# Kernel tuning notes

Measured on AMD Instinct MI355X. Metric: run time of the kernel, lower is better.

The kernel has to match this reference:

```python
import jax, jax.numpy as jnp
import numpy as np

B, S, N = 1024, 64, 256
ODE_UNFOLDS = 12
EPS = 1e-8
ELAPSED_TIME = 1.0

def _uniform(key, shape, lo, hi):
    return jax.random.uniform(key, shape, jnp.float32, lo, hi)

def setup_inputs() -> dict:
    key = jax.random.key(0)
    ks = jax.random.split(key, 16)
    return {
        "inputs": jax.random.normal(ks[0], (B, S), jnp.float32),
        "state": jax.random.normal(ks[1], (B, N), jnp.float32),
        "gleak": _uniform(ks[2], (N,), 0.001, 1.0),
        "vleak": _uniform(ks[3], (N,), -0.2, 0.2),
        "cm": _uniform(ks[4], (N,), 0.4, 0.6),
        "w": _uniform(ks[5], (N, N), 0.001, 1.0),
        "sigma": _uniform(ks[6], (N, N), 3.0, 8.0),
        "mu": _uniform(ks[7], (N, N), 0.3, 0.8),
        "erev": jnp.where(jax.random.bernoulli(ks[8], 0.5, (N, N)), 1.0, -1.0).astype(jnp.float32),
        "sensory_w": _uniform(ks[9], (S, N), 0.001, 1.0),
        "sensory_sigma": _uniform(ks[10], (S, N), 3.0, 8.0),
        "sensory_mu": _uniform(ks[11], (S, N), 0.3, 0.8),
        "sensory_erev": jnp.where(jax.random.bernoulli(ks[12], 0.5, (S, N)), 1.0, -1.0).astype(jnp.float32),
        "sparsity_mask": jax.random.bernoulli(ks[13], 0.5, (N, N)).astype(jnp.float32),
        "sensory_sparsity_mask": jax.random.bernoulli(ks[14], 0.5, (S, N)).astype(jnp.float32),
    }

def _sig(v_pre, mu, sigma):
    # v_pre: [B, pre] -> [B, pre, 1]; mu/sigma: [pre, post] -> broadcast to [B, pre, post]
    return jax.nn.sigmoid(sigma[None] * (v_pre[:, :, None] - mu[None]))

def reference(inputs, state, gleak, vleak, cm, w, sigma, mu, erev,
              sensory_w, sensory_sigma, sensory_mu, sensory_erev,
              sparsity_mask, sensory_sparsity_mask):
    # sensory pre-activation (computed once): [B, S, N]
    sensory_act = jax.nn.softplus(sensory_w) * _sig(inputs, sensory_mu, sensory_sigma)
    sensory_act = sensory_act * sensory_sparsity_mask
    w_num_sensory = jnp.sum(sensory_act * sensory_erev, axis=1)  # [B, N]
    w_den_sensory = jnp.sum(sensory_act, axis=1)                 # [B, N]

    cm_t = jax.nn.softplus(cm) / (ELAPSED_TIME / ODE_UNFOLDS)    # [N]
    w_param = jax.nn.softplus(w)                                 # [N, N]
    gleak_sp = jax.nn.softplus(gleak)                            # [N]

    def step(v_pre, _):
        w_act = w_param * _sig(v_pre, mu, sigma) * sparsity_mask  # [B, N, N]
        w_num = jnp.sum(w_act * erev, axis=1) + w_num_sensory     # [B, N]
        w_den = jnp.sum(w_act, axis=1) + w_den_sensory            # [B, N]
        numerator = cm_t * v_pre + gleak_sp * vleak + w_num
        denominator = cm_t + gleak_sp + w_den
        return numerator / (denominator + EPS), None

    v_pre, _ = jax.lax.scan(step, state, None, length=ODE_UNFOLDS)
    return v_pre
```

## Files before the change

kernel.cpp:

```cpp
#include <hip/hip_runtime.h>
#include <math.h>

#define B_TOT   1024
#define S_DIM   64
#define N_DIM   256
#define UNFOLDS 12
#define EPSF    1e-8f
#define L2E     1.4426950408889634f
#define KMAX    256
#define ECLAMP  1073741824.0f

#if defined(__has_builtin)
#  if __has_builtin(__builtin_amdgcn_exp2f)
#    define FEXP2(x) __builtin_amdgcn_exp2f(x)
#  endif
#  if __has_builtin(__builtin_amdgcn_rcpf)
#    define FRCP(x) __builtin_amdgcn_rcpf(x)
#  endif
#endif
#ifndef FEXP2
__device__ __forceinline__ float __fexp2_asm(float x){ float r; asm("v_exp_f32 %0, %1" : "=v"(r) : "v"(x)); return r; }
#  define FEXP2(x) __fexp2_asm(x)
#endif
#ifndef FRCP
__device__ __forceinline__ float __frcp_asm(float x){ float r; asm("v_rcp_f32 %0, %1" : "=v"(r) : "v"(x)); return r; }
#  define FRCP(x) __frcp_asm(x)
#endif

__device__ __forceinline__ float softplus_f(float x) {
    return log1pf(expf(x));
}

#define MQUAD(p, v0, v1, v2, v3, m0, d0, m1, d1, m2, d2, m3, d3)            \
    {                                                                       \
        float _t0 = fmaf(p.x, v0, p.y);                                     \
        float _t1 = fmaf(p.x, v1, p.y);                                     \
        float _t2 = fmaf(p.x, v2, p.y);                                     \
        float _t3 = fmaf(p.x, v3, p.y);                                     \
        float _e0 = fminf(FEXP2(_t0), ECLAMP);                              \
        float _e1 = fminf(FEXP2(_t1), ECLAMP);                              \
        float _e2 = fminf(FEXP2(_t2), ECLAMP);                              \
        float _e3 = fminf(FEXP2(_t3), ECLAMP);                              \
        float _a0 = 1.0f + _e0, _a1 = 1.0f + _e1;                           \
        float _a2 = 1.0f + _e2, _a3 = 1.0f + _e3;                           \
        float _b01 = _a0 * _a1, _b23 = _a2 * _a3;                           \
        float _ip   = FRCP(_b01 * _b23);                                    \
        float _ip01 = _b23 * _ip, _ip23 = _b01 * _ip;                       \
        float _r0 = _a1 * _ip01, _r1 = _a0 * _ip01;                         \
        float _r2 = _a3 * _ip23, _r3 = _a2 * _ip23;                         \
        m0 = fmaf(p.w, _r0, m0); d0 = fmaf(p.z, _r0, d0);                   \
        m1 = fmaf(p.w, _r1, m1); d1 = fmaf(p.z, _r1, d1);                   \
        m2 = fmaf(p.w, _r2, m2); d2 = fmaf(p.z, _r2, d2);                   \
        m3 = fmaf(p.w, _r3, m3); d3 = fmaf(p.z, _r3, d3);                   \
    }

__global__ void ltc_precompute_s(const float* __restrict__ gleak, const float* __restrict__ vleak,
                                 const float* __restrict__ cm,
                                 const float* __restrict__ sw,    const float* __restrict__ ssig,
                                 const float* __restrict__ smu,   const float* __restrict__ serev,
                                 const float* __restrict__ smask,
                                 float4* __restrict__ s4, float4* __restrict__ pj,
                                 int* __restrict__ wmax)
{
    const int idx = blockIdx.x * blockDim.x + threadIdx.x;
    if (idx < S_DIM * N_DIM) {
        float we = softplus_f(sw[idx]) * smask[idx];
        float sg = ssig[idx];
        float4 o;
        o.x = -L2E * sg;
        o.y =  L2E * sg * smu[idx];
        o.z =  we;
        o.w =  we * serev[idx];
        s4[idx] = o;
    }
    if (idx < N_DIM) {
        float g = softplus_f(gleak[idx]);
        float4 o;
        o.x = softplus_f(cm[idx]) * (float)UNFOLDS;
        o.y = g;
        o.z = g * vleak[idx];
        o.w = 0.0f;
        pj[idx] = o;
    }
    if (idx < 4) wmax[idx] = 0;
}

__global__ __launch_bounds__(256)
void ltc_compact(const float* __restrict__ w,    const float* __restrict__ sigma,
                 const float* __restrict__ mu,   const float* __restrict__ erev,
                 const float* __restrict__ mask,
                 float4* __restrict__ pc, unsigned short* __restrict__ pofs,
                 int* __restrict__ wmax)
{
    const int j = blockIdx.x;
    const int i = threadIdx.x;
    const int idx = i * N_DIM + j;

    const float mk = mask[idx];
    const bool live = mk > 0.0f;
    float we = softplus_f(w[idx]) * mk;
    float sg = sigma[idx];
    float4 o;
    o.x = -L2E * sg;
    o.y =  L2E * sg * mu[idx];
    o.z =  we;
    o.w =  we * erev[idx];

    const int lane = i & 63, wv = i >> 6;
    const unsigned long long ball = __ballot(live);
    const int lpre = __popcll(ball & ((1ull << lane) - 1ull));
    __shared__ int wcnt[4];
    if (lane == 0) wcnt[wv] = __popcll(ball);
    __syncthreads();
    int base = 0;
    #pragma unroll
    for (int ww = 0; ww < 4; ++ww) base += (ww < wv) ? wcnt[ww] : 0;
    const int total = wcnt[0] + wcnt[1] + wcnt[2] + wcnt[3];

    if (live) {
        const int pos = base + lpre;
        pc[pos * N_DIM + j] = o;
        pofs[pos * N_DIM + j] = (unsigned short)(i << 4);
    }
    for (int k = total + i; k < KMAX; k += 256) {
        pc[k * N_DIM + j] = make_float4(0.f, 0.f, 0.f, 0.f);
        pofs[k * N_DIM + j] = 0;
    }
    if (i == 0) atomicMax(&wmax[j >> 6], total);
}

__global__ __launch_bounds__(1024, 2)
void ltc_main(const float* __restrict__ inputs, const float* __restrict__ state,
              const float4* __restrict__ pc, const unsigned short* __restrict__ pofs,
              const int* __restrict__ wmax,
              const float4* __restrict__ s4, const float4* __restrict__ pj,
              float* __restrict__ out)
{
    __shared__ float4 v4[N_DIM];
    __shared__ float4 pnum[4][N_DIM];
    __shared__ float4 pden[4][N_DIM];
    __shared__ float  in_lds[4][S_DIM];

    const int tid = threadIdx.x;
    const int j   = tid & (N_DIM - 1);
    const int q   = tid >> 8;
    const int b0  = blockIdx.x << 2;

    ((float*)v4)[(j << 2) + q] = state[(b0 + q) * N_DIM + j];
    if (tid < 4 * S_DIM) in_lds[tid >> 6][tid & 63] = inputs[b0 * S_DIM + tid];

    const float4 c = pj[j];
    const float cmt = c.x, gl = c.y, glv = c.z;
    const float cg  = cmt + gl + EPSF;

    const int wl  = wmax[j >> 6];
    const int U4w = ((wl + 31) & ~31) >> 2;
    __syncthreads();

    float n0 = 0.f, n1 = 0.f, n2 = 0.f, n3 = 0.f;
    float d0 = 0.f, d1 = 0.f, d2 = 0.f, d3 = 0.f;
    {
        const float4* __restrict__ sr = s4 + (q << 4) * N_DIM + j;
        const int sb = q << 4;
        #pragma unroll 4
        for (int s = 0; s < 16; ++s) {
            const float4 p = sr[s * N_DIM];
            const float i0 = in_lds[0][sb + s];
            const float i1 = in_lds[1][sb + s];
            const float i2 = in_lds[2][sb + s];
            const float i3 = in_lds[3][sb + s];
            MQUAD(p, i0, i1, i2, i3, n0, d0, n1, d1, n2, d2, n3, d3)
        }
    }
    pnum[q][j] = make_float4(n0, n1, n2, n3);
    pden[q][j] = make_float4(d0, d1, d2, d3);
    __syncthreads();

    float4 sn = make_float4(0.f, 0.f, 0.f, 0.f);
    float4 sd = make_float4(0.f, 0.f, 0.f, 0.f);
    #pragma unroll
    for (int qq = 0; qq < 4; ++qq) {
        const float4 a = pnum[qq][j], b = pden[qq][j];
        sn.x += a.x; sn.y += a.y; sn.z += a.z; sn.w += a.w;
        sd.x += b.x; sd.y += b.y; sd.z += b.z; sd.w += b.w;
    }
    __syncthreads();

    const float4*         __restrict__ pr = pc   + (q * U4w) * N_DIM + j;
    const unsigned short* __restrict__ po = pofs + (q * U4w) * N_DIM + j;

    #pragma unroll 1
    for (int step = 0; step < UNFOLDS; ++step) {
        float m0 = 0.f, m1 = 0.f, m2 = 0.f, m3 = 0.f;
        float h0 = 0.f, h1 = 0.f, h2 = 0.f, h3 = 0.f;

        #pragma unroll 8
        for (int t = 0; t < U4w; ++t) {
            const float4 p   = pr[t * N_DIM];
            const int    off = (int)po[t * N_DIM];
            const float4 vv  = *(const float4*)((const char*)v4 + off);
            MQUAD(p, vv.x, vv.y, vv.z, vv.w, m0, h0, m1, h1, m2, h2, m3, h3)
        }

        const float4 vo = v4[j];
        pnum[q][j] = make_float4(m0, m1, m2, m3);
        pden[q][j] = make_float4(h0, h1, h2, h3);
        __syncthreads();

        float4 tn = sn, td = sd;
        #pragma unroll
        for (int qq = 0; qq < 4; ++qq) {
            const float4 a = pnum[qq][j], b = pden[qq][j];
            tn.x += a.x; tn.y += a.y; tn.z += a.z; tn.w += a.w;
            td.x += b.x; td.y += b.y; td.z += b.z; td.w += b.w;
        }
        const float g0 = cg + td.x, g1 = cg + td.y;
        const float g2 = cg + td.z, g3 = cg + td.w;
        const float b01 = g0 * g1, b23 = g2 * g3;
        const float ip   = FRCP(b01 * b23);
        const float ip01 = b23 * ip, ip23 = b01 * ip;
        float4 vn;
        vn.x = (fmaf(cmt, vo.x, glv) + tn.x) * (g1 * ip01);
        vn.y = (fmaf(cmt, vo.y, glv) + tn.y) * (g0 * ip01);
        vn.z = (fmaf(cmt, vo.z, glv) + tn.z) * (g3 * ip23);
        vn.w = (fmaf(cmt, vo.w, glv) + tn.w) * (g2 * ip23);
        v4[j] = vn;
        __syncthreads();
    }

    out[(b0 + q) * N_DIM + j] = ((const float*)v4)[(j << 2) + q];
}

extern "C" void kernel_launch(void* const* d_in, const int* in_sizes, int n_in,
                              void* d_out, int out_size, void* d_ws, size_t ws_size,
                              hipStream_t stream)
{
    const float* inputs = (const float*)d_in[0];
    const float* state  = (const float*)d_in[1];
    const float* gleak  = (const float*)d_in[2];
    const float* vleak  = (const float*)d_in[3];
    const float* cm     = (const float*)d_in[4];
    const float* w      = (const float*)d_in[5];
    const float* sigma  = (const float*)d_in[6];
    const float* mu     = (const float*)d_in[7];
    const float* erev   = (const float*)d_in[8];
    const float* sw     = (const float*)d_in[9];
    const float* ssig   = (const float*)d_in[10];
    const float* smu    = (const float*)d_in[11];
    const float* serev  = (const float*)d_in[12];
    const float* mask   = (const float*)d_in[13];
    const float* smask  = (const float*)d_in[14];

    float4* s4 = (float4*)d_ws;
    float4* pj = s4 + S_DIM * N_DIM;
    float4* pc = pj + N_DIM;
    unsigned short* pofs = (unsigned short*)(pc + KMAX * N_DIM);
    int* wmax = (int*)(pofs + KMAX * N_DIM);

    ltc_precompute_s<<<(S_DIM * N_DIM + 255) / 256, 256, 0, stream>>>(
        gleak, vleak, cm, sw, ssig, smu, serev, smask, s4, pj, wmax);

    ltc_compact<<<N_DIM, 256, 0, stream>>>(w, sigma, mu, erev, mask, pc, pofs, wmax);

    ltc_main<<<B_TOT / 4, 1024, 0, stream>>>(inputs, state, pc, pofs, wmax,
                                             s4, pj, (float*)d_out);
}
```

Measured before the change: 158.1 us.

## Sort postsynaptic columns by sparsity count to balance per-wave loop lengths

Adds a count kernel and a single-block bitonic sort that order postsynaptic columns by the number of live synapses. Sensory parameters, per-neuron constants and the compacted synapse arrays are then stored in sorted slot order. Each thread loops over its own column's quarter length instead of a per-64-column max rounded up to 32, so wavefronts contain columns of similar length and do less padded work. The cost is two extra small launches, a permuted LDS write pattern, and a smaller unroll factor in the inner loop.

```diff
diff --git a/kernel.cpp b/kernel.cpp
--- a/kernel.cpp
+++ b/kernel.cpp
@@ -54,16 +54,56 @@
         m3 = fmaf(p.w, _r3, m3); d3 = fmaf(p.z, _r3, d3);                   \
     }
 
+__global__ __launch_bounds__(256)
+void ltc_count(const float* __restrict__ mask, int* __restrict__ cnt)
+{
+    const int col = blockIdx.x, i = threadIdx.x;
+    const bool live = mask[i * N_DIM + col] > 0.0f;
+    const int lane = i & 63, wv = i >> 6;
+    const unsigned long long ball = __ballot(live);
+    __shared__ int wcnt[4];
+    if (lane == 0) wcnt[wv] = __popcll(ball);
+    __syncthreads();
+    if (i == 0) cnt[col] = wcnt[0] + wcnt[1] + wcnt[2] + wcnt[3];
+}
+
+__global__ __launch_bounds__(256)
+void ltc_sort(const int* __restrict__ cnt, int* __restrict__ perm,
+              int* __restrict__ slotof, int* __restrict__ qm)
+{
+    __shared__ int key[N_DIM];
+    const int t = threadIdx.x;
+    key[t] = (cnt[t] << 8) | t;
+    __syncthreads();
+    for (int k = 2; k <= N_DIM; k <<= 1) {
+        for (int jj = k >> 1; jj > 0; jj >>= 1) {
+            const int ixj = t ^ jj;
+            if (ixj > t) {
+                const int a = key[t], b = key[ixj];
+                const bool asc = (t & k) == 0;
+                if (asc ? (a > b) : (a < b)) { key[t] = b; key[ixj] = a; }
+            }
+            __syncthreads();
+        }
+    }
+    const int kk = key[t];
+    const int col = kk & 255;
+    perm[t] = col;
+    slotof[col] = t;
+    qm[t] = ((kk >> 8) + 3) >> 2;
+}
+
 __global__ void ltc_precompute_s(const float* __restrict__ gleak, const float* __restrict__ vleak,
                                  const float* __restrict__ cm,
                                  const float* __restrict__ sw,    const float* __restrict__ ssig,
                                  const float* __restrict__ smu,   const float* __restrict__ serev,
-                                 const float* __restrict__ smask,
-                                 float4* __restrict__ s4, float4* __restrict__ pj,
-                                 int* __restrict__ wmax)
+                                 const float* __restrict__ smask, const int* __restrict__ slotof,
+                                 float4* __restrict__ s4, float4* __restrict__ pj)
 {
     const int idx = blockIdx.x * blockDim.x + threadIdx.x;
     if (idx < S_DIM * N_DIM) {
+        const int col = idx & (N_DIM - 1), s = idx >> 8;
+        const int slot = slotof[col];
         float we = softplus_f(sw[idx]) * smask[idx];
         float sg = ssig[idx];
         float4 o;
@@ -71,30 +111,30 @@
         o.y =  L2E * sg * smu[idx];
         o.z =  we;
         o.w =  we * serev[idx];
-        s4[idx] = o;
+        s4[s * N_DIM + slot] = o;
     }
     if (idx < N_DIM) {
+        const int slot = slotof[idx];
         float g = softplus_f(gleak[idx]);
         float4 o;
         o.x = softplus_f(cm[idx]) * (float)UNFOLDS;
         o.y = g;
         o.z = g * vleak[idx];
         o.w = 0.0f;
-        pj[idx] = o;
-    }
-    if (idx < 4) wmax[idx] = 0;
+        pj[slot] = o;
+    }
 }
 
 __global__ __launch_bounds__(256)
 void ltc_compact(const float* __restrict__ w,    const float* __restrict__ sigma,
                  const float* __restrict__ mu,   const float* __restrict__ erev,
-                 const float* __restrict__ mask,
-                 float4* __restrict__ pc, unsigned short* __restrict__ pofs,
-                 int* __restrict__ wmax)
-{
-    const int j = blockIdx.x;
-    const int i = threadIdx.x;
-    const int idx = i * N_DIM + j;
+                 const float* __restrict__ mask, const int* __restrict__ slotof,
+                 float4* __restrict__ pc, unsigned short* __restrict__ pofs)
+{
+    const int col = blockIdx.x;
+    const int i   = threadIdx.x;
+    const int idx = i * N_DIM + col;
+    const int slot = slotof[col];
 
     const float mk = mask[idx];
     const bool live = mk > 0.0f;
@@ -119,20 +159,20 @@
 
     if (live) {
         const int pos = base + lpre;
-        pc[pos * N_DIM + j] = o;
-        pofs[pos * N_DIM + j] = (unsigned short)(i << 4);
-    }
-    for (int k = total + i; k < KMAX; k += 256) {
-        pc[k * N_DIM + j] = make_float4(0.f, 0.f, 0.f, 0.f);
-        pofs[k * N_DIM + j] = 0;
-    }
-    if (i == 0) atomicMax(&wmax[j >> 6], total);
+        pc[pos * N_DIM + slot] = o;
+        pofs[pos * N_DIM + slot] = (unsigned short)(i << 4);
+    }
+    const int K4 = (total + 3) & ~3;
+    for (int k = total + i; k < K4; k += 256) {
+        pc[k * N_DIM + slot] = make_float4(0.f, 0.f, 0.f, 0.f);
+        pofs[k * N_DIM + slot] = 0;
+    }
 }
 
 __global__ __launch_bounds__(1024, 2)
 void ltc_main(const float* __restrict__ inputs, const float* __restrict__ state,
               const float4* __restrict__ pc, const unsigned short* __restrict__ pofs,
-              const int* __restrict__ wmax,
+              const int* __restrict__ perm, const int* __restrict__ qm,
               const float4* __restrict__ s4, const float4* __restrict__ pj,
               float* __restrict__ out)
 {
@@ -141,26 +181,25 @@
     __shared__ float4 pden[4][N_DIM];
     __shared__ float  in_lds[4][S_DIM];
 
-    const int tid = threadIdx.x;
-    const int j   = tid & (N_DIM - 1);
-    const int q   = tid >> 8;
-    const int b0  = blockIdx.x << 2;
-
-    ((float*)v4)[(j << 2) + q] = state[(b0 + q) * N_DIM + j];
+    const int tid  = threadIdx.x;
+    const int slot = tid & (N_DIM - 1);
+    const int q    = tid >> 8;
+    const int b0   = blockIdx.x << 2;
+
+    ((float*)v4)[(slot << 2) + q] = state[(b0 + q) * N_DIM + slot];
     if (tid < 4 * S_DIM) in_lds[tid >> 6][tid & 63] = inputs[b0 * S_DIM + tid];
 
-    const float4 c = pj[j];
+    const int   col = perm[slot];
+    const int   myq = qm[slot];
+    const float4 c  = pj[slot];
     const float cmt = c.x, gl = c.y, glv = c.z;
     const float cg  = cmt + gl + EPSF;
-
-    const int wl  = wmax[j >> 6];
-    const int U4w = ((wl + 31) & ~31) >> 2;
     __syncthreads();
 
     float n0 = 0.f, n1 = 0.f, n2 = 0.f, n3 = 0.f;
     float d0 = 0.f, d1 = 0.f, d2 = 0.f, d3 = 0.f;
     {
-        const float4* __restrict__ sr = s4 + (q << 4) * N_DIM + j;
+        const float4* __restrict__ sr = s4 + (q << 4) * N_DIM + slot;
         const int sb = q << 4;
         #pragma unroll 4
         for (int s = 0; s < 16; ++s) {
@@ -172,45 +211,45 @@
             MQUAD(p, i0, i1, i2, i3, n0, d0, n1, d1, n2, d2, n3, d3)
         }
     }
-    pnum[q][j] = make_float4(n0, n1, n2, n3);
-    pden[q][j] = make_float4(d0, d1, d2, d3);
+    pnum[q][slot] = make_float4(n0, n1, n2, n3);
+    pden[q][slot] = make_float4(d0, d1, d2, d3);
     __syncthreads();
 
     float4 sn = make_float4(0.f, 0.f, 0.f, 0.f);
     float4 sd = make_float4(0.f, 0.f, 0.f, 0.f);
     #pragma unroll
     for (int qq = 0; qq < 4; ++qq) {
-        const float4 a = pnum[qq][j], b = pden[qq][j];
+        const float4 a = pnum[qq][slot], b = pden[qq][slot];
         sn.x += a.x; sn.y += a.y; sn.z += a.z; sn.w += a.w;
         sd.x += b.x; sd.y += b.y; sd.z += b.z; sd.w += b.w;
     }
     __syncthreads();
 
-    const float4*         __restrict__ pr = pc   + (q * U4w) * N_DIM + j;
-    const unsigned short* __restrict__ po = pofs + (q * U4w) * N_DIM + j;
+    const float4*         __restrict__ pr = pc   + (q * myq) * N_DIM + slot;
+    const unsigned short* __restrict__ po = pofs + (q * myq) * N_DIM + slot;
 
     #pragma unroll 1
     for (int step = 0; step < UNFOLDS; ++step) {
         float m0 = 0.f, m1 = 0.f, m2 = 0.f, m3 = 0.f;
         float h0 = 0.f, h1 = 0.f, h2 = 0.f, h3 = 0.f;
 
-        #pragma unroll 8
-        for (int t = 0; t < U4w; ++t) {
+        #pragma unroll 4
+        for (int t = 0; t < myq; ++t) {
             const float4 p   = pr[t * N_DIM];
             const int    off = (int)po[t * N_DIM];
             const float4 vv  = *(const float4*)((const char*)v4 + off);
             MQUAD(p, vv.x, vv.y, vv.z, vv.w, m0, h0, m1, h1, m2, h2, m3, h3)
         }
 
-        const float4 vo = v4[j];
-        pnum[q][j] = make_float4(m0, m1, m2, m3);
-        pden[q][j] = make_float4(h0, h1, h2, h3);
+        const float4 vo = v4[col];
+        pnum[q][slot] = make_float4(m0, m1, m2, m3);
+        pden[q][slot] = make_float4(h0, h1, h2, h3);
         __syncthreads();
 
         float4 tn = sn, td = sd;
         #pragma unroll
         for (int qq = 0; qq < 4; ++qq) {
-            const float4 a = pnum[qq][j], b = pden[qq][j];
+            const float4 a = pnum[qq][slot], b = pden[qq][slot];
             tn.x += a.x; tn.y += a.y; tn.z += a.z; tn.w += a.w;
             td.x += b.x; td.y += b.y; td.z += b.z; td.w += b.w;
         }
@@ -224,11 +263,11 @@
         vn.y = (fmaf(cmt, vo.y, glv) + tn.y) * (g0 * ip01);
         vn.z = (fmaf(cmt, vo.z, glv) + tn.z) * (g3 * ip23);
         vn.w = (fmaf(cmt, vo.w, glv) + tn.w) * (g2 * ip23);
-        v4[j] = vn;
+        v4[col] = vn;
         __syncthreads();
     }
 
-    out[(b0 + q) * N_DIM + j] = ((const float*)v4)[(j << 2) + q];
+    out[(b0 + q) * N_DIM + col] = ((const float*)v4)[(col << 2) + q];
 }
 
 extern "C" void kernel_launch(void* const* d_in, const int* in_sizes, int n_in,
@@ -255,13 +294,19 @@
     float4* pj = s4 + S_DIM * N_DIM;
     float4* pc = pj + N_DIM;
     unsigned short* pofs = (unsigned short*)(pc + KMAX * N_DIM);
-    int* wmax = (int*)(pofs + KMAX * N_DIM);
+    int* cnt    = (int*)(pofs + KMAX * N_DIM);
+    int* perm   = cnt + N_DIM;
+    int* slotof = perm + N_DIM;
+    int* qm     = slotof + N_DIM;
+
+    ltc_count<<<N_DIM, 256, 0, stream>>>(mask, cnt);
+    ltc_sort<<<1, N_DIM, 0, stream>>>(cnt, perm, slotof, qm);
 
     ltc_precompute_s<<<(S_DIM * N_DIM + 255) / 256, 256, 0, stream>>>(
-        gleak, vleak, cm, sw, ssig, smu, serev, smask, s4, pj, wmax);
-
-    ltc_compact<<<N_DIM, 256, 0, stream>>>(w, sigma, mu, erev, mask, pc, pofs, wmax);
-
-    ltc_main<<<B_TOT / 4, 1024, 0, stream>>>(inputs, state, pc, pofs, wmax,
+        gleak, vleak, cm, sw, ssig, smu, serev, smask, slotof, s4, pj);
+
+    ltc_compact<<<N_DIM, 256, 0, stream>>>(w, sigma, mu, erev, mask, slotof, pc, pofs);
+
+    ltc_main<<<B_TOT / 4, 1024, 0, stream>>>(inputs, state, pc, pofs, perm, qm,
                                              s4, pj, (float*)d_out);
 }
```

New measurement: 168.3 us, median of 5. 1.06x slower.
